# Optimization experiments

Hardware: AMD Instinct MI355X
Metric: run time of the kernel (lower is better)

The kernel has to match this reference:

```python
import jax, jax.numpy as jnp
import numpy as np

EMBED_DIM = 1024
NUM_HEADS = 16
HEAD_DIM = EMBED_DIM // NUM_HEADS


def setup_inputs() -> dict:
    key = jax.random.key(0)
    k_x, k_wqkv, k_bqkv, k_wo, k_bo = jax.random.split(key, 5)
    B, T, C = 8, 1024, EMBED_DIM
    s = 1.0 / np.sqrt(C)
    return {
        "x": jax.random.normal(k_x, (B, T, C), dtype=jnp.float32),
        "W_qkv": jax.random.uniform(k_wqkv, (C, 3 * C), minval=-s, maxval=s, dtype=jnp.float32),
        "b_qkv": jax.random.uniform(k_bqkv, (3 * C,), minval=-s, maxval=s, dtype=jnp.float32),
        "W_out": jax.random.uniform(k_wo, (C, C), minval=-s, maxval=s, dtype=jnp.float32),
        "b_out": jax.random.uniform(k_bo, (C,), minval=-s, maxval=s, dtype=jnp.float32),
    }


def reference(x, W_qkv, b_qkv, W_out, b_out):
    B, T, C = x.shape
    H, D = NUM_HEADS, HEAD_DIM
    qkv = x @ W_qkv + b_qkv                      # [B,T,3C]
    q, k, v = jnp.split(qkv, 3, axis=-1)
    q = q.reshape(B, T, H, D).transpose(0, 2, 1, 3)  # [B,H,T,D]
    k = k.reshape(B, T, H, D).transpose(0, 2, 1, 3)
    v = v.reshape(B, T, H, D).transpose(0, 2, 1, 3)
    scores = jnp.einsum("bhqd,bhkd->bhqk", q, k) / np.sqrt(D).astype(np.float32)
    causal = jnp.tril(jnp.ones((T, T), dtype=bool))
    scores = jnp.where(causal[None, None], scores, -jnp.inf)
    attn = jax.nn.softmax(scores, axis=-1)       # dropout is identity in eval
    out = jnp.einsum("bhqk,bhkd->bhqd", attn, v)
    out = out.transpose(0, 2, 1, 3).reshape(B, T, C)
    return out @ W_out + b_out
```

## Files before the change

### kernel.cpp

```cpp
#include <hip/hip_runtime.h>
#include <hip/hip_bf16.h>
#include <cstdint>

using bf16 = __hip_bfloat16;
typedef short short8 __attribute__((ext_vector_type(8)));
typedef float floatx4 __attribute__((ext_vector_type(4)));

#define QSCALE 0.1803368801111601f

__device__ __forceinline__ void async_load16(const bf16* g, bf16* l) {
    __builtin_amdgcn_global_load_lds(
        (const __attribute__((address_space(1))) uint32_t*)g,
        (__attribute__((address_space(3))) uint32_t*)l, 16, 0, 0);
}

__device__ __forceinline__ void bar_vm4_lgkm0() {
    asm volatile("s_waitcnt vmcnt(4) lgkmcnt(0)\ns_barrier" ::: "memory");
}
__device__ __forceinline__ void bar_vm0_lgkm0() {
    asm volatile("s_waitcnt vmcnt(0) lgkmcnt(0)\ns_barrier" ::: "memory");
}

__device__ __forceinline__ uint32_t pack2(float a, float b) {
    union { bf16 h[2]; uint32_t u; } p;
    p.h[0] = __float2bfloat16(a);
    p.h[1] = __float2bfloat16(b);
    return p.u;
}

__device__ __forceinline__ float fast_exp2(float x) {
    float r;
    asm("v_exp_f32 %0, %1" : "=v"(r) : "v"(x));
    return r;
}

__global__ __launch_bounds__(256)
void cvt_bf16_kernel(const float* __restrict__ in, bf16* __restrict__ out) {
    const int i = (blockIdx.x * 256 + threadIdx.x) * 4;
    const float4 v = *(const float4*)(in + i);
    bf16 o[4] = {__float2bfloat16(v.x), __float2bfloat16(v.y),
                 __float2bfloat16(v.z), __float2bfloat16(v.w)};
    *(ushort4*)(out + i) = *(ushort4*)o;
}

__global__ __launch_bounds__(256)
void transpose_cvt2_kernel(const float* __restrict__ inA, bf16* __restrict__ outA,
                           const float* __restrict__ inB, bf16* __restrict__ outB) {
    __shared__ float tile[32][33];
    const int tx = threadIdx.x & 31, ty = threadIdx.x >> 5;
    const bool isB = blockIdx.x >= 96;
    const float* __restrict__ in = isB ? inB : inA;
    bf16* __restrict__ out = isB ? outB : outA;
    const int C = isB ? 1024 : 3072;
    const int bx = isB ? blockIdx.x - 96 : blockIdx.x;
    const int c0 = bx * 32, r0 = blockIdx.y * 32;
    const int R = 1024;
    #pragma unroll
    for (int i = 0; i < 32; i += 8)
        tile[ty + i][tx] = in[(size_t)(r0 + ty + i) * C + c0 + tx];
    __syncthreads();
    #pragma unroll
    for (int i = 0; i < 32; i += 8)
        out[(size_t)(c0 + ty + i) * R + r0 + tx] = __float2bfloat16(tile[tx][ty + i]);
}

template <int MODE>
__global__ __launch_bounds__(256, 3)
void gemm_bt_kernel(const bf16* __restrict__ A, const bf16* __restrict__ Bt,
                    const float* __restrict__ bias, int K,
                    bf16* __restrict__ q_ws, bf16* __restrict__ k_ws,
                    bf16* __restrict__ vt_ws, float* __restrict__ out, int N) {
    __shared__ bf16 As[3][128 * 32];
    __shared__ bf16 Bs[3][128 * 32];
    const int tid = threadIdx.x;
    const int wave = tid >> 6, lane = tid & 63;
    const int ln = lane & 15, quad = lane >> 4;
    const int wm = wave & 1, wn = wave >> 1;
    const int m0 = blockIdx.y * 128, n0 = blockIdx.x * 128;

    floatx4 acc[4][4] = {};
    const int nkt = K >> 5;

    #pragma unroll
    for (int t = 0; t < 2; ++t) {
        const int k0 = t << 5;
        #pragma unroll
        for (int c = 0; c < 2; ++c) {
            const int e = (c * 256 + tid) * 8;
            const int row = e >> 5;
            const int gch = ((((e >> 3) & 3) ^ ((row >> 1) & 3)) << 3);
            async_load16(A + (size_t)(m0 + row) * K + k0 + gch,
                         &As[t][(c * 256 + wave * 64) * 8]);
        }
        #pragma unroll
        for (int c = 0; c < 2; ++c) {
            const int e = (c * 256 + tid) * 8;
            const int row = e >> 5;
            const int gch = ((((e >> 3) & 3) ^ ((row >> 1) & 3)) << 3);
            async_load16(Bt + (size_t)(n0 + row) * K + k0 + gch,
                         &Bs[t][(c * 256 + wave * 64) * 8]);
        }
    }

    for (int kt = 0; kt < nkt; ++kt) {
        const int cur = kt % 3;
        if (kt + 1 < nkt) bar_vm4_lgkm0();
        else              bar_vm0_lgkm0();

        if (kt + 2 < nkt) {
            const int nxt = (kt + 2) % 3;
            const int k0 = (kt + 2) << 5;
            #pragma unroll
            for (int c = 0; c < 2; ++c) {
                const int e = (c * 256 + tid) * 8;
                const int row = e >> 5;
                const int gch = ((((e >> 3) & 3) ^ ((row >> 1) & 3)) << 3);
                async_load16(A + (size_t)(m0 + row) * K + k0 + gch,
                             &As[nxt][(c * 256 + wave * 64) * 8]);
            }
            #pragma unroll
            for (int c = 0; c < 2; ++c) {
                const int e = (c * 256 + tid) * 8;
                const int row = e >> 5;
                const int gch = ((((e >> 3) & 3) ^ ((row >> 1) & 3)) << 3);
                async_load16(Bt + (size_t)(n0 + row) * K + k0 + gch,
                             &Bs[nxt][(c * 256 + wave * 64) * 8]);
            }
        }

        const int chq = ((quad ^ ((ln >> 1) & 3)) << 3);
        short8 af[4], bfr[4];
        #pragma unroll
        for (int i = 0; i < 4; ++i) {
            af[i]  = *(const short8*)&As[cur][(wm * 64 + i * 16 + ln) * 32 + chq];
            bfr[i] = *(const short8*)&Bs[cur][(wn * 64 + i * 16 + ln) * 32 + chq];
        }
        #pragma unroll
        for (int mi = 0; mi < 4; ++mi)
            #pragma unroll
            for (int ni = 0; ni < 4; ++ni)
                acc[mi][ni] = __builtin_amdgcn_mfma_f32_16x16x32_bf16(
                    af[mi], bfr[ni], acc[mi][ni], 0, 0, 0);
    }

    #pragma unroll
    for (int ni = 0; ni < 4; ++ni) {
        const int col = n0 + wn * 64 + ni * 16 + ln;
        const float bv = bias[col];
        if (MODE == 0) {
            const int which = col >> 10;
            const int cc = col & 1023;
            const int h = cc >> 6, d = cc & 63;
            #pragma unroll
            for (int mi = 0; mi < 4; ++mi) {
                const int rowb = m0 + wm * 64 + mi * 16 + quad * 4;
                if (which == 2) {
                    const int bb = rowb >> 10, t = rowb & 1023;
                    const int tl = t & 63;
                    const int tt = (t & ~63) + ((((tl >> 3) ^ (d & 7)) << 3) | (tl & 7));
                    uint2 w2 = { pack2(acc[mi][ni][0] + bv, acc[mi][ni][1] + bv),
                                 pack2(acc[mi][ni][2] + bv, acc[mi][ni][3] + bv) };
                    *(uint2*)&vt_ws[((size_t)(bb * 16 + h) * 64 + d) * 1024 + tt] = w2;
                } else {
                    bf16* dst = (which == 0) ? q_ws : k_ws;
                    #pragma unroll
                    for (int r = 0; r < 4; ++r) {
                        const int row = rowb + r;
                        const int bb = row >> 10, t = row & 1023;
                        float v = acc[mi][ni][r] + bv;
                        if (which == 0) v *= QSCALE;
                        const int dd = (((d >> 3) ^ (t & 7)) << 3) | (d & 7);
                        dst[((size_t)(bb * 16 + h) * 1024 + t) * 64 + dd] =
                            __float2bfloat16(v);
                    }
                }
            }
        } else {
            #pragma unroll
            for (int mi = 0; mi < 4; ++mi) {
                const int rowb = m0 + wm * 64 + mi * 16 + quad * 4;
                #pragma unroll
                for (int r = 0; r < 4; ++r)
                    out[(size_t)(rowb + r) * N + col] = acc[mi][ni][r] + bv;
            }
        }
    }
}

__global__ __launch_bounds__(256, 3)
void attn_kernel(const bf16* __restrict__ Q, const bf16* __restrict__ K,
                 const bf16* __restrict__ Vt, bf16* __restrict__ O) {
    constexpr int T = 1024;
    __shared__ bf16 Ps[128 * 64];

    const int lid = blockIdx.x + (blockIdx.y << 3);
    const int bh = ((lid & 7) << 4) | ((lid >> 3) & 15);
    const int jt = 7 - (lid >> 7);
    const int q0 = jt << 7;

    const int tid = threadIdx.x;
    const int wave = tid >> 6, lane = tid & 63;
    const int ln = lane & 15, quad = lane >> 4;
    const int b = bh >> 4, h = bh & 15;

    const bf16* Qg = Q + ((size_t)bh * T + q0) * 64;
    const bf16* Kg = K + (size_t)bh * T * 64;
    const bf16* Vg = Vt + (size_t)bh * 64 * T;

    short8 bq[2][2];
    #pragma unroll
    for (int qs = 0; qs < 2; ++qs)
        #pragma unroll
        for (int ks = 0; ks < 2; ++ks) {
            const int row = wave * 16 + qs * 64 + ln;
            const int ch = (ks * 4 + quad) ^ (ln & 7);
            bq[qs][ks] = *(const short8*)(Qg + (size_t)row * 64 + ch * 8);
        }

    floatx4 oacc[2][4] = {};
    float rl[2] = {0.f, 0.f};
    const int qb0 = q0 + wave * 16;
    const int qb1 = qb0 + 64;
    const int nktw = ((qb1 + 15) >> 6) + 1;

    for (int kt = 0; kt < nktw; ++kt) {
        const int k0 = kt << 6;
        const bool tail = (k0 + 63 > qb0);

        floatx4 sacc[2][4] = {};
        __builtin_amdgcn_s_setprio(1);
        #pragma unroll
        for (int nj = 0; nj < 4; ++nj) {
            short8 ak[2];
            #pragma unroll
            for (int ks = 0; ks < 2; ++ks) {
                const int trow = k0 + nj * 16 + ln;
                const int ch = (ks * 4 + quad) ^ (ln & 7);
                ak[ks] = *(const short8*)(Kg + (size_t)trow * 64 + ch * 8);
            }
            #pragma unroll
            for (int qs = 0; qs < 2; ++qs) {
                const int qb = qs ? qb1 : qb0;
                if (k0 + nj * 16 > qb + 15) continue;
                #pragma unroll
                for (int ks = 0; ks < 2; ++ks)
                    sacc[qs][nj] = __builtin_amdgcn_mfma_f32_16x16x32_bf16(
                        ak[ks], bq[qs][ks], sacc[qs][nj], 0, 0, 0);
            }
        }
        __builtin_amdgcn_s_setprio(0);

        if (tail) {
            #pragma unroll
            for (int qs = 0; qs < 2; ++qs) {
                const int qq = (qs ? qb1 : qb0) + ln;
                #pragma unroll
                for (int nj = 0; nj < 4; ++nj)
                    #pragma unroll
                    for (int r = 0; r < 4; ++r) {
                        const int kk = k0 + nj * 16 + quad * 4 + r;
                        if (kk > qq) sacc[qs][nj][r] = -1e30f;
                    }
            }
        }

        #pragma unroll
        for (int qs = 0; qs < 2; ++qs) {
            float rs = 0.f;
            const int qrow = wave * 16 + qs * 64 + ln;
            #pragma unroll
            for (int nj = 0; nj < 4; ++nj) {
                float p[4];
                #pragma unroll
                for (int r = 0; r < 4; ++r) {
                    p[r] = fast_exp2(sacc[qs][nj][r]);
                    rs += p[r];
                }
                const int kcol = nj * 16 + quad * 4;
                const int ch = (kcol >> 3) ^ (qrow & 7);
                uint2 w2 = { pack2(p[0], p[1]), pack2(p[2], p[3]) };
                *(uint2*)&Ps[qrow * 64 + ch * 8 + (kcol & 7)] = w2;
            }
            rl[qs] += rs;
        }

        __builtin_amdgcn_s_setprio(1);
        #pragma unroll
        for (int ks4 = 0; ks4 < 2; ++ks4) {
            short8 bp[2];
            #pragma unroll
            for (int qs = 0; qs < 2; ++qs) {
                const int qrow = wave * 16 + qs * 64 + ln;
                const int chp = (ks4 * 4 + quad) ^ (ln & 7);
                bp[qs] = *(const short8*)&Ps[qrow * 64 + chp * 8];
            }
            #pragma unroll
            for (int dt = 0; dt < 4; ++dt) {
                const int d = dt * 16 + ln;
                const int ch = (ks4 * 4 + quad) ^ (ln & 7);
                const short8 av = *(const short8*)(Vg + (size_t)d * T + k0 + ch * 8);
                #pragma unroll
                for (int qs = 0; qs < 2; ++qs)
                    oacc[qs][dt] = __builtin_amdgcn_mfma_f32_16x16x32_bf16(
                        av, bp[qs], oacc[qs][dt], 0, 0, 0);
            }
        }
        __builtin_amdgcn_s_setprio(0);
    }

    #pragma unroll
    for (int qs = 0; qs < 2; ++qs) {
        float l = rl[qs];
        l += __shfl_xor(l, 16, 64);
        l += __shfl_xor(l, 32, 64);
        const float inv = 1.0f / l;
        const int t = q0 + qs * 64 + wave * 16 + ln;
        const size_t rowb = ((size_t)b * 1024 + t) * 1024 + h * 64;
        #pragma unroll
        for (int dt = 0; dt < 4; ++dt) {
            uint2 w2 = { pack2(oacc[qs][dt][0] * inv, oacc[qs][dt][1] * inv),
                         pack2(oacc[qs][dt][2] * inv, oacc[qs][dt][3] * inv) };
            *(uint2*)&O[rowb + dt * 16 + quad * 4] = w2;
        }
    }
}

extern "C" void kernel_launch(void* const* d_in, const int* in_sizes, int n_in,
                              void* d_out, int out_size, void* d_ws, size_t ws_size,
                              hipStream_t stream) {
    const float* x     = (const float*)d_in[0];
    const float* W_qkv = (const float*)d_in[1];
    const float* b_qkv = (const float*)d_in[2];
    const float* W_out = (const float*)d_in[3];
    const float* b_out = (const float*)d_in[4];
    float* out = (float*)d_out;

    char* ws = (char*)d_ws;
    const size_t MB = 1u << 20;
    bf16* x_bf   = (bf16*)(ws + 0);
    bf16* wqkv_t = (bf16*)(ws + 16 * MB);
    bf16* wout_t = (bf16*)(ws + 22 * MB);
    bf16* q_ws   = (bf16*)(ws + 24 * MB);
    bf16* k_ws   = (bf16*)(ws + 40 * MB);
    bf16* vt_ws  = (bf16*)(ws + 56 * MB);
    bf16* ao_ws  = (bf16*)(ws + 72 * MB);

    cvt_bf16_kernel<<<8192, 256, 0, stream>>>(x, x_bf);
    transpose_cvt2_kernel<<<dim3(128, 32), 256, 0, stream>>>(W_qkv, wqkv_t, W_out, wout_t);

    gemm_bt_kernel<0><<<dim3(24, 64), 256, 0, stream>>>(
        x_bf, wqkv_t, b_qkv, 1024, q_ws, k_ws, vt_ws, nullptr, 3072);

    attn_kernel<<<dim3(8, 128), 256, 0, stream>>>(q_ws, k_ws, vt_ws, ao_ws);

    gemm_bt_kernel<1><<<dim3(8, 64), 256, 0, stream>>>(
        ao_ws, wout_t, b_out, 1024, nullptr, nullptr, nullptr, out, 1024);
}
```

Measured before the change: 239.5 us.

## Prefetch K and V tiles into registers in attention; drop GEMM LDS swizzle

```diff
diff --git a/kernel.cpp b/kernel.cpp
--- a/kernel.cpp
+++ b/kernel.cpp
@@ -87,17 +87,13 @@
         #pragma unroll
         for (int c = 0; c < 2; ++c) {
             const int e = (c * 256 + tid) * 8;
-            const int row = e >> 5;
-            const int gch = ((((e >> 3) & 3) ^ ((row >> 1) & 3)) << 3);
-            async_load16(A + (size_t)(m0 + row) * K + k0 + gch,
+            async_load16(A + (size_t)(m0 + (e >> 5)) * K + k0 + (e & 31),
                          &As[t][(c * 256 + wave * 64) * 8]);
         }
         #pragma unroll
         for (int c = 0; c < 2; ++c) {
             const int e = (c * 256 + tid) * 8;
-            const int row = e >> 5;
-            const int gch = ((((e >> 3) & 3) ^ ((row >> 1) & 3)) << 3);
-            async_load16(Bt + (size_t)(n0 + row) * K + k0 + gch,
+            async_load16(Bt + (size_t)(n0 + (e >> 5)) * K + k0 + (e & 31),
                          &Bs[t][(c * 256 + wave * 64) * 8]);
         }
     }
@@ -113,27 +109,22 @@
             #pragma unroll
             for (int c = 0; c < 2; ++c) {
                 const int e = (c * 256 + tid) * 8;
-                const int row = e >> 5;
-                const int gch = ((((e >> 3) & 3) ^ ((row >> 1) & 3)) << 3);
-                async_load16(A + (size_t)(m0 + row) * K + k0 + gch,
+                async_load16(A + (size_t)(m0 + (e >> 5)) * K + k0 + (e & 31),
                              &As[nxt][(c * 256 + wave * 64) * 8]);
             }
             #pragma unroll
             for (int c = 0; c < 2; ++c) {
                 const int e = (c * 256 + tid) * 8;
-                const int row = e >> 5;
-                const int gch = ((((e >> 3) & 3) ^ ((row >> 1) & 3)) << 3);
-                async_load16(Bt + (size_t)(n0 + row) * K + k0 + gch,
+                async_load16(Bt + (size_t)(n0 + (e >> 5)) * K + k0 + (e & 31),
                              &Bs[nxt][(c * 256 + wave * 64) * 8]);
             }
         }
 
-        const int chq = ((quad ^ ((ln >> 1) & 3)) << 3);
         short8 af[4], bfr[4];
         #pragma unroll
         for (int i = 0; i < 4; ++i) {
-            af[i]  = *(const short8*)&As[cur][(wm * 64 + i * 16 + ln) * 32 + chq];
-            bfr[i] = *(const short8*)&Bs[cur][(wn * 64 + i * 16 + ln) * 32 + chq];
+            af[i]  = *(const short8*)&As[cur][(wm * 64 + i * 16 + ln) * 32 + quad * 8];
+            bfr[i] = *(const short8*)&Bs[cur][(wn * 64 + i * 16 + ln) * 32 + quad * 8];
         }
         #pragma unroll
         for (int mi = 0; mi < 4; ++mi)
@@ -207,6 +198,7 @@
     const bf16* Kg = K + (size_t)bh * T * 64;
     const bf16* Vg = Vt + (size_t)bh * 64 * T;
 
+    const int chq = ((quad) ^ (ln & 7)) * 8;
     short8 bq[2][2];
     #pragma unroll
     for (int qs = 0; qs < 2; ++qs)
@@ -223,6 +215,16 @@
     const int qb1 = qb0 + 64;
     const int nktw = ((qb1 + 15) >> 6) + 1;
 
+    short8 akr[4][2];
+    #pragma unroll
+    for (int nj = 0; nj < 4; ++nj)
+        #pragma unroll
+        for (int ks = 0; ks < 2; ++ks) {
+            const int trow = nj * 16 + ln;
+            const int ch = (ks * 4 + quad) ^ (ln & 7);
+            akr[nj][ks] = *(const short8*)(Kg + (size_t)trow * 64 + ch * 8);
+        }
+
     for (int kt = 0; kt < nktw; ++kt) {
         const int k0 = kt << 6;
         const bool tail = (k0 + 63 > qb0);
@@ -231,13 +233,6 @@
         __builtin_amdgcn_s_setprio(1);
         #pragma unroll
         for (int nj = 0; nj < 4; ++nj) {
-            short8 ak[2];
-            #pragma unroll
-            for (int ks = 0; ks < 2; ++ks) {
-                const int trow = k0 + nj * 16 + ln;
-                const int ch = (ks * 4 + quad) ^ (ln & 7);
-                ak[ks] = *(const short8*)(Kg + (size_t)trow * 64 + ch * 8);
-            }
             #pragma unroll
             for (int qs = 0; qs < 2; ++qs) {
                 const int qb = qs ? qb1 : qb0;
@@ -245,10 +240,32 @@
                 #pragma unroll
                 for (int ks = 0; ks < 2; ++ks)
                     sacc[qs][nj] = __builtin_amdgcn_mfma_f32_16x16x32_bf16(
-                        ak[ks], bq[qs][ks], sacc[qs][nj], 0, 0, 0);
+                        akr[nj][ks], bq[qs][ks], sacc[qs][nj], 0, 0, 0);
             }
         }
         __builtin_amdgcn_s_setprio(0);
+
+        short8 av[2][4];
+        #pragma unroll
+        for (int ks4 = 0; ks4 < 2; ++ks4)
+            #pragma unroll
+            for (int dt = 0; dt < 4; ++dt) {
+                const int d = dt * 16 + ln;
+                const int ch = (ks4 * 4 + quad) ^ (ln & 7);
+                av[ks4][dt] = *(const short8*)(Vg + (size_t)d * T + k0 + ch * 8);
+            }
+
+        if (kt + 1 < nktw) {
+            const int kn = k0 + 64;
+            #pragma unroll
+            for (int nj = 0; nj < 4; ++nj)
+                #pragma unroll
+                for (int ks = 0; ks < 2; ++ks) {
+                    const int trow = kn + nj * 16 + ln;
+                    const int ch = (ks * 4 + quad) ^ (ln & 7);
+                    akr[nj][ks] = *(const short8*)(Kg + (size_t)trow * 64 + ch * 8);
+                }
+        }
 
         if (tail) {
             #pragma unroll
@@ -296,13 +313,10 @@
             }
             #pragma unroll
             for (int dt = 0; dt < 4; ++dt) {
-                const int d = dt * 16 + ln;
-                const int ch = (ks4 * 4 + quad) ^ (ln & 7);
-                const short8 av = *(const short8*)(Vg + (size_t)d * T + k0 + ch * 8);
                 #pragma unroll
                 for (int qs = 0; qs < 2; ++qs)
                     oacc[qs][dt] = __builtin_amdgcn_mfma_f32_16x16x32_bf16(
-                        av, bp[qs], oacc[qs][dt], 0, 0, 0);
+                        av[ks4][dt], bp[qs], oacc[qs][dt], 0, 0, 0);
             }
         }
         __builtin_amdgcn_s_setprio(0);
```

Result: slower. 289.5 us (+20.9%).
